# Kernel tuning notes

Hardware: AMD Instinct MI355X
Metric: run time of the kernel (lower is better)

The kernel has to match this reference:

```python
import jax, jax.numpy as jnp
import numpy as np

MODEL_DIM = 1024
HEAD_DIM = 64
NUM_HEADS = 16
FF_DIM = 4 * MODEL_DIM
ROT_DIM = 32  # max(head_dim // 2, 32)
FUSED = (NUM_HEADS * HEAD_DIM,) * 3 + (FF_DIM,) * 2
B, S = 2, 2048


def rotate_half(x):
    x1, x2 = jnp.split(x, 2, axis=-1)
    return jnp.concatenate([-x2, x1], axis=-1)


def rope_freqs(seq_len, dim=ROT_DIM, max_period=10000.0):
    inv_freq = 1.0 / max_period ** (jnp.arange(0, dim, 2, dtype=jnp.float32) / dim)
    freqs = jnp.arange(seq_len, dtype=jnp.float32)[:, None] * inv_freq[None, :]
    return jnp.concatenate([freqs, freqs], axis=-1)  # [S, dim]


def setup_inputs() -> dict:
    key = jax.random.key(0)
    ks = jax.random.split(key, 10)
    d = MODEL_DIM
    s_in = (sum(FUSED) ** -0.5)
    return {
        "inputs": jax.random.normal(ks[0], (B, S, d), jnp.float32),
        "time_embeds": jax.random.normal(ks[1], (B, 1, d), jnp.float32),
        "ln_w": jnp.ones((d,), jnp.float32),
        "ln_b": jnp.zeros((d,), jnp.float32),
        "cond_w": jax.random.normal(ks[2], (d, 2 * d), jnp.float32) * (d ** -0.5),
        "cond_b": jnp.zeros((2 * d,), jnp.float32),
        "w_in": jax.random.normal(ks[3], (d, sum(FUSED)), jnp.float32) * (d ** -0.5),
        "w_attn": jax.random.normal(ks[4], (NUM_HEADS * HEAD_DIM, d), jnp.float32) * ((NUM_HEADS * HEAD_DIM) ** -0.5),
        "w_ff": jax.random.normal(ks[5], (FF_DIM, d), jnp.float32) * (FF_DIM ** -0.5),
        "b_ff": jnp.zeros((d,), jnp.float32),
    }


def reference(inputs, time_embeds, ln_w, ln_b, cond_w, cond_b, w_in, w_attn, w_ff, b_ff):
    # LayerNorm
    mu = jnp.mean(inputs, axis=-1, keepdims=True)
    var = jnp.mean(jnp.square(inputs - mu), axis=-1, keepdims=True)
    units = (inputs - mu) * jax.lax.rsqrt(var + 1e-5) * ln_w + ln_b

    # FiLM conditioning
    cond = jax.nn.silu(time_embeds) @ cond_w + cond_b  # [B,1,2D]
    scale, bias = jnp.split(cond, 2, axis=-1)
    units = (1.0 + scale) * units + bias

    # Fused projection -> q, k, v, ff, ff_gate
    proj = units @ w_in
    splits = np.cumsum(FUSED)[:-1].tolist()
    q, k, v, ff, ff_gate = jnp.split(proj, splits, axis=-1)

    def split_heads(x):  # [B,S,H*hd] -> [B,H,S,hd]
        return x.reshape(B, S, NUM_HEADS, HEAD_DIM).transpose(0, 2, 1, 3)

    q, k, v = split_heads(q), split_heads(k), split_heads(v)

    # Rotary on first ROT_DIM dims of q, k
    freqs = rope_freqs(S)  # [S, ROT_DIM]
    cos, sin = jnp.cos(freqs), jnp.sin(freqs)

    def rope(x):
        xl, xr = x[..., :ROT_DIM], x[..., ROT_DIM:]
        xl = xl * cos + rotate_half(xl) * sin
        return jnp.concatenate([xl, xr], axis=-1)

    q, k = rope(q), rope(k)

    # Attention (full score matrix, manual softmax, as original)
    score = jnp.einsum("bhsd,bhSd->bhsS", q, k) * (HEAD_DIM ** -0.5)
    weight = jax.nn.softmax(score, axis=-1)
    attn = jnp.einsum("bhsS,bhSd->bhsd", weight, v)
    concat = attn.transpose(0, 2, 1, 3).reshape(B, S, NUM_HEADS * HEAD_DIM)
    attn_out = concat @ w_attn

    # GeGLU FF
    ff_out = (ff * jax.nn.gelu(ff_gate, approximate=True)) @ w_ff + b_ff

    return inputs + attn_out + ff_out
```

## Files before the change

kernel.cpp:

```cpp
#include <hip/hip_runtime.h>
#include <hip/hip_bf16.h>

typedef __attribute__((ext_vector_type(8))) __bf16 bf16x8;
typedef __attribute__((ext_vector_type(4))) float f32x4;
typedef unsigned short u16;
typedef unsigned int u32;

#define DMODEL 1024
#define SLEN   2048
#define NPROJ  11264
#define NFUSE  5120
#define MROWS  4096

__device__ __forceinline__ float b2f(u16 u){ u32 v=((u32)u)<<16; float f; __builtin_memcpy(&f,&v,4); return f; }
__device__ __forceinline__ u16 f2b(float f){ u32 u; __builtin_memcpy(&u,&f,4); u32 r=u+0x7fffu+((u>>16)&1u); return (u16)(r>>16); }
__device__ __forceinline__ float fexp2(float x){ return __builtin_amdgcn_exp2f(x); }

__device__ __forceinline__ void gload16(const void* g, void* l){
  __builtin_amdgcn_global_load_lds((__attribute__((address_space(1))) u32*)g,
                                   (__attribute__((address_space(3))) u32*)l, 16, 0, 0);
}

#define BARR asm volatile("s_barrier" ::: "memory")

template<int REMAP>
__global__ __launch_bounds__(256) void k_transpose(const float* __restrict__ src, int N,
                                                   u16* __restrict__ dst, int ldd, int coloff){
  __shared__ float tile[32][33];
  int n0 = blockIdx.x*32, k0 = blockIdx.y*32;
  int tx = threadIdx.x & 31, ty = threadIdx.x >> 5;
  int srccol;
  if (REMAP && (n0 + tx) >= 3072){
    int c = n0 + tx - 3072;
    int q = c >> 5, o = c & 31;
    srccol = (o < 16) ? (3072 + 16*q + o) : (7168 + 16*q + (o-16));
  } else srccol = n0 + tx;
  #pragma unroll
  for (int r=0;r<4;r++)
    tile[ty*4+r][tx] = src[(size_t)(k0+ty*4+r)*N + srccol];
  __syncthreads();
  #pragma unroll
  for (int r=0;r<4;r++){
    int n = ty*4+r;
    dst[(size_t)(n0+n)*ldd + coloff + k0 + tx] = f2b(tile[tx][n]);
  }
}

__global__ __launch_bounds__(256) void k_rope_table(float* __restrict__ tab){
  int idx = blockIdx.x*256 + threadIdx.x;
  if (idx >= SLEN*16) return;
  int s = idx >> 4, i = idx & 15;
  float inv = powf(10000.f, -(float)i/16.f);
  float f = (float)s * inv;
  tab[s*32 + i]      = cosf(f);
  tab[s*32 + 16 + i] = sinf(f);
}

__global__ __launch_bounds__(256) void k_cond(const float* __restrict__ te, const float* __restrict__ cw,
                                              const float* __restrict__ cb, float* __restrict__ cond){
  __shared__ float sl[DMODEL];
  int b = blockIdx.y, t = threadIdx.x;
  for (int i=t;i<DMODEL;i+=256){ float x = te[b*DMODEL+i]; sl[i] = x/(1.f+expf(-x)); }
  __syncthreads();
  int n = blockIdx.x*256 + t;
  float acc = 0.f;
  for (int k=0;k<DMODEL;k++) acc += sl[k]*cw[(size_t)k*2048 + n];
  cond[b*2048+n] = acc + cb[n];
}

__global__ __launch_bounds__(256) void k_ln(const float* __restrict__ x, const float* __restrict__ lw,
                                            const float* __restrict__ lb, const float* __restrict__ cond,
                                            u16* __restrict__ units){
  int row = blockIdx.x; int b = row >> 11;
  int t = threadIdx.x;
  const float4 v = *(const float4*)(x + (size_t)row*DMODEL + t*4);
  float s = v.x+v.y+v.z+v.w;
  float q = v.x*v.x+v.y*v.y+v.z*v.z+v.w*v.w;
  #pragma unroll
  for (int off=32; off; off>>=1){ s += __shfl_xor(s,off); q += __shfl_xor(q,off); }
  __shared__ float red[8];
  int w = t>>6, l = t&63;
  if (l==0){ red[w]=s; red[4+w]=q; }
  __syncthreads();
  float S = red[0]+red[1]+red[2]+red[3];
  float Q = red[4]+red[5]+red[6]+red[7];
  float mu = S*(1.f/1024.f);
  float var = Q*(1.f/1024.f) - mu*mu;
  float rstd = rsqrtf(var + 1e-5f);
  int c0 = t*4;
  u16 o[4];
  const float* vf = (const float*)&v;
  #pragma unroll
  for (int i=0;i<4;i++){
    int c = c0+i;
    float nrm = (vf[i]-mu)*rstd*lw[c] + lb[c];
    float outv = (1.f + cond[b*2048 + c])*nrm + cond[b*2048 + 1024 + c];
    o[i] = f2b(outv);
  }
  u32 p0 = (u32)o[0] | ((u32)o[1]<<16);
  u32 p1 = (u32)o[2] | ((u32)o[3]<<16);
  uint2 pk; pk.x = p0; pk.y = p1;
  *(uint2*)(units + (size_t)row*DMODEL + c0) = pk;
}

__global__ __launch_bounds__(512,2) void k_gemm8_proj(
    const u16* __restrict__ A, const u16* __restrict__ Bt, const float* __restrict__ tab,
    u16* __restrict__ qh, u16* __restrict__ kh, u16* __restrict__ vq, u16* __restrict__ afinal)
{
  __shared__ __attribute__((aligned(16))) u16 lds[65536];
  int t = threadIdx.x, w = t>>6, l = t&63;
  int wr = w>>2, wc = w&3;
  int lane16 = l&15, lg = l>>4;

  int nbx = gridDim.x;
  int wg = blockIdx.y*nbx + blockIdx.x;
  int nwg = nbx*gridDim.y;
  int cpx = nwg>>3;
  int swz = (wg&7)*cpx + (wg>>3);
  int bx = swz % nbx, by = swz / nbx;

  size_t m0 = (size_t)by*256, n0 = (size_t)bx*256;
  const u16* Ag = A + m0*DMODEL;
  const u16* Bg = Bt + n0*DMODEL;

  f32x4 zero = {0.f,0.f,0.f,0.f};
  f32x4 acc[8][4];
  #pragma unroll
  for (int i=0;i<8;i++)
    #pragma unroll
    for (int j=0;j<4;j++) acc[i][j] = zero;

  bf16x8 a[8][2], bv[4][2];

  auto STAGEA = [&](int u, int h){
    const u16* src = Ag + (size_t)(h*128)*DMODEL + u*64;
    char* dst = (char*)lds + ((u&1)<<16) + (h<<14);
    #pragma unroll
    for (int i=0;i<2;i++){
      int cid = i*512 + t;
      int r = cid>>3, s2 = cid&7;
      gload16(src + (size_t)r*DMODEL + ((s2 ^ (r&7))<<3), dst + ((i*512 + w*64)<<4));
    }
  };
  auto STAGEB = [&](int u, int h){
    const u16* src = Bg + (size_t)(h*128)*DMODEL + u*64;
    char* dst = (char*)lds + ((u&1)<<16) + 32768 + (h<<14);
    #pragma unroll
    for (int i=0;i<2;i++){
      int cid = i*512 + t;
      int r = cid>>3, s2 = cid&7;
      gload16(src + (size_t)r*DMODEL + ((s2 ^ (r&7))<<3), dst + ((i*512 + w*64)<<4));
    }
  };
  auto LDA4 = [&](int u, int fi0){
    const char* base = (const char*)lds + ((u&1)<<16) + (wr<<14);
    #pragma unroll
    for (int i=0;i<4;i++){
      int r = (fi0+i)*16 + lane16;
      #pragma unroll
      for (int kk=0;kk<2;kk++){
        int c = kk*4 + lg;
        a[fi0+i][kk] = *(const bf16x8*)(base + r*128 + ((c ^ (r&7))<<4));
      }
    }
  };
  auto LDB2 = [&](int u, int fj0){
    const char* base = (const char*)lds + ((u&1)<<16) + 32768 + ((wc>>1)<<14);
    #pragma unroll
    for (int j=0;j<2;j++){
      int r = (wc&1)*64 + (fj0+j)*16 + lane16;
      #pragma unroll
      for (int kk=0;kk<2;kk++){
        int c = kk*4 + lg;
        bv[fj0+j][kk] = *(const bf16x8*)(base + r*128 + ((c ^ (r&7))<<4));
      }
    }
  };
  auto MMQ = [&](int I0, int J0){
    #pragma unroll
    for (int i=0;i<4;i++)
      #pragma unroll
      for (int j=0;j<2;j++)
        #pragma unroll
        for (int kk=0;kk<2;kk++)
          acc[I0+i][J0+j] = __builtin_amdgcn_mfma_f32_16x16x32_bf16(
              a[I0+i][kk], bv[J0+j][kk], acc[I0+i][J0+j], 0,0,0);
  };

  const int T = DMODEL/64;
  STAGEA(0,0); STAGEA(0,1); STAGEB(0,0); STAGEB(0,1); STAGEA(1,0); STAGEA(1,1);
  asm volatile("s_waitcnt vmcnt(4)" ::: "memory");
  BARR;

  for (int u=0; u<T; ++u){
    LDA4(u,0); LDB2(u,0);
    if (u+1<T) STAGEB(u+1,0);
    BARR;
    __builtin_amdgcn_s_setprio(1);
    MMQ(0,0);
    __builtin_amdgcn_s_setprio(0);
    BARR;
    LDA4(u,4);
    if (u+1<T) STAGEB(u+1,1);
    BARR;
    __builtin_amdgcn_s_setprio(1);
    MMQ(4,0);
    __builtin_amdgcn_s_setprio(0);
    BARR;
    LDB2(u,2);
    if (u+2<T) STAGEA(u+2,0);
    BARR;
    __builtin_amdgcn_s_setprio(1);
    MMQ(0,2);
    __builtin_amdgcn_s_setprio(0);
    BARR;
    if (u+2<T) STAGEA(u+2,1);
    BARR;
    __builtin_amdgcn_s_setprio(1);
    MMQ(4,2);
    __builtin_amdgcn_s_setprio(0);
    asm volatile("s_waitcnt vmcnt(4)" ::: "memory");
    BARR;
  }

  int region = (n0 < 3072) ? (int)(n0>>10) : 3;
  if (region<=1){
    u16* dst = (region==0)? qh : kh;
    float sc = (region==0)? 0.125f*1.44269504f : 1.0f;
    int h = (int)((n0 & 1023)>>6) + wc;
    int d = lane16;
    #pragma unroll
    for (int i=0;i<8;i++){
      #pragma unroll
      for (int r=0;r<4;r++){
        int row = (int)m0 + wr*128 + i*16 + lg*4 + r;
        int bb = row>>11, s = row&2047;
        float cs = tab[s*32+d], sn = tab[s*32+16+d];
        float x0 = acc[i][0][r], x1 = acc[i][1][r];
        size_t base = ((size_t)(bb*16+h)*SLEN + s)*64;
        dst[base+d]    = f2b((x0*cs - x1*sn)*sc);
        dst[base+16+d] = f2b((x1*cs + x0*sn)*sc);
        dst[base+32+d] = f2b(acc[i][2][r]*sc);
        dst[base+48+d] = f2b(acc[i][3][r]*sc);
      }
    }
  } else if (region==2){
    #pragma unroll
    for (int i=0;i<8;i++)
      #pragma unroll
      for (int j=0;j<4;j++){
        int cv = (int)(n0-2048) + wc*64 + j*16 + lane16;
        #pragma unroll
        for (int r=0;r<4;r++){
          int row = (int)m0 + wr*128 + i*16 + lg*4 + r;
          vq[(size_t)row*DMODEL + cv] = f2b(acc[i][j][r]);
        }
      }
  } else {
    int fbase = (int)((n0-3072)>>1) + wc*32 + lane16;
    #pragma unroll
    for (int i=0;i<8;i++)
      #pragma unroll
      for (int p=0;p<2;p++){
        int col = 1024 + fbase + p*16;
        #pragma unroll
        for (int r=0;r<4;r++){
          int row = (int)m0 + wr*128 + i*16 + lg*4 + r;
          float fv = acc[i][2*p][r];
          float gv = acc[i][2*p+1][r];
          float tz = 0.7978845608f*(gv + 0.044715f*gv*gv*gv);
          float th = 1.f - 2.f/(__expf(2.f*tz)+1.f);
          afinal[(size_t)row*NFUSE + col] = f2b(fv * 0.5f*gv*(1.f+th));
        }
      }
  }
}

template<int BM,int BN,int WM,int WN,int NBUF,int MINW,int EPI>
__global__ __launch_bounds__(WM*WN*64, MINW) void k_gemm_pipe(
    const u16* __restrict__ A, const u16* __restrict__ Bt, int K, int lda, int ldb,
    const float* __restrict__ tab, u16* __restrict__ qh, u16* __restrict__ kh,
    u16* __restrict__ vq, u16* __restrict__ afinal, float* __restrict__ pb)
{
  constexpr int THREADS = WM*WN*64;
  constexpr int MR = BM/WM/16, NR = BN/WN/16;
  constexpr int BUFE = (BM+BN)*32;
  __shared__ __attribute__((aligned(16))) u16 lds[NBUF*BUFE];
  int t = threadIdx.x, w = t>>6, l = t&63;
  int wr = w/WN, wc = w%WN;
  int lane16 = l&15, lg = l>>4;

  int nbx = gridDim.x;
  int wg = blockIdx.y*nbx + blockIdx.x;
  int nwg = nbx*gridDim.y;
  int cpx = nwg>>3;
  int swz = (wg&7)*cpx + (wg>>3);
  int bx = swz % nbx, by = swz / nbx;

  size_t m0 = (size_t)by*BM, n0 = (size_t)bx*BN;
  int koff = (EPI==1) ? blockIdx.z*1280 : 0;
  const u16* Ag = A + m0*lda + koff;
  const u16* Bg = Bt + n0*ldb + koff;

  f32x4 zero = {0.f,0.f,0.f,0.f};
  f32x4 acc[MR][NR];
  #pragma unroll
  for (int i=0;i<MR;i++)
    #pragma unroll
    for (int j=0;j<NR;j++) acc[i][j] = zero;

  const int ntiles = K/32;

  auto STAGE = [&](int tt, int buf){
    int k0 = tt*32;
    char* Ad = (char*)lds + (size_t)buf*(BUFE*2);
    char* Bd = Ad + BM*64;
    #pragma unroll
    for (int i=0;i<2;i++){
      int s = i*THREADS + t;
      int r = s>>2, g = s&3;
      int src = (g ^ ((r>>1)&3))*8;
      gload16(Ag + (size_t)r*lda + k0 + src, Ad + (i*THREADS + w*64)*16);
      gload16(Bg + (size_t)r*ldb + k0 + src, Bd + (i*THREADS + w*64)*16);
    }
  };

  #pragma unroll
  for (int p=0;p<NBUF-1;p++) STAGE(p, p);

  int cur = 0;
  for (int kt=0; kt<ntiles; ++kt){
    int rem = ntiles-1-kt;
    if (rem>=1)      asm volatile("s_waitcnt vmcnt(4)" ::: "memory");
    else             asm volatile("s_waitcnt vmcnt(0)" ::: "memory");
    __builtin_amdgcn_s_barrier();
    const u16* As = lds + (size_t)cur*BUFE;
    const u16* Bs = As + BM*32;
    bf16x8 af[MR], bf[NR];
    #pragma unroll
    for (int i=0;i<MR;i++){
      int r = wr*(MR*16) + i*16 + lane16;
      int g = lg ^ ((r>>1)&3);
      af[i] = *(const bf16x8*)(As + r*32 + g*8);
    }
    #pragma unroll
    for (int j=0;j<NR;j++){
      int r = wc*(NR*16) + j*16 + lane16;
      int g = lg ^ ((r>>1)&3);
      bf[j] = *(const bf16x8*)(Bs + r*32 + g*8);
    }
    int st = kt + NBUF-1;
    if (st < ntiles) STAGE(st, (cur==0)?(NBUF-1):(cur-1));
    __builtin_amdgcn_s_setprio(1);
    #pragma unroll
    for (int i=0;i<MR;i++)
      #pragma unroll
      for (int j=0;j<NR;j++)
        acc[i][j] = __builtin_amdgcn_mfma_f32_16x16x32_bf16(af[i], bf[j], acc[i][j], 0,0,0);
    __builtin_amdgcn_s_setprio(0);
    __builtin_amdgcn_sched_barrier(0);
    cur = (cur+1==NBUF)?0:(cur+1);
  }

  if constexpr (EPI==1){
    float* pbs = pb + (size_t)blockIdx.z*MROWS*DMODEL;
    #pragma unroll
    for (int i=0;i<MR;i++)
      #pragma unroll
      for (int j=0;j<NR;j++){
        int col = (int)n0 + wc*(NR*16) + j*16 + lane16;
        #pragma unroll
        for (int r=0;r<4;r++){
          int row = (int)m0 + wr*(MR*16) + i*16 + lg*4 + r;
          pbs[(size_t)row*DMODEL + col] = acc[i][j][r];
        }
      }
  }
}

__global__ __launch_bounds__(256) void k_reduce(const float* __restrict__ pb, const float* __restrict__ resid,
                                                const float* __restrict__ bias, float* __restrict__ out){
  size_t i4 = ((size_t)blockIdx.x*256 + threadIdx.x)*4;
  float4 a0 = *(const float4*)(pb + i4);
  float4 a1 = *(const float4*)(pb + (size_t)MROWS*DMODEL + i4);
  float4 a2 = *(const float4*)(pb + (size_t)2*MROWS*DMODEL + i4);
  float4 a3 = *(const float4*)(pb + (size_t)3*MROWS*DMODEL + i4);
  float4 rv = *(const float4*)(resid + i4);
  float4 bv = *(const float4*)(bias + (i4 & 1023));
  float4 o;
  o.x = a0.x+a1.x+a2.x+a3.x+rv.x+bv.x;
  o.y = a0.y+a1.y+a2.y+a3.y+rv.y+bv.y;
  o.z = a0.z+a1.z+a2.z+a3.z+rv.z+bv.z;
  o.w = a0.w+a1.w+a2.w+a3.w+rv.w+bv.w;
  *(float4*)(out + i4) = o;
}

__global__ __launch_bounds__(256) void k_vtrans(const u16* __restrict__ vq, u16* __restrict__ vt){
  int b = blockIdx.z, h = blockIdx.y, s0 = blockIdx.x*64;
  int t = threadIdx.x;
  __shared__ u16 vt_lds[64][72];
  int sl = t>>2, quad = t&3;
  const u16* prow = vq + (size_t)(b*SLEN + s0 + sl)*DMODEL + h*64;
  #pragma unroll
  for (int i=0;i<16;i++){
    int d = quad*16+i;
    vt_lds[d][sl] = prow[d];
  }
  __syncthreads();
  int d = t>>2, sg = t&3;
  size_t base = ((size_t)(b*16+h)*64 + d)*SLEN + s0 + sg*16;
  #pragma unroll
  for (int i=0;i<16;i++)
    vt[base + i] = vt_lds[d][sg*16+i];
}

#define M0SHIFT 20.0f
__global__ __launch_bounds__(256,3) void k_attn(const u16* __restrict__ qh, const u16* __restrict__ kh,
                                                const u16* __restrict__ vt,
                                                float* __restrict__ op, float* __restrict__ lsum){
  __shared__ __attribute__((aligned(16))) u16 Klds[2][64*64];
  __shared__ __attribute__((aligned(16))) u16 Vlds[2][64*64];
  __shared__ __attribute__((aligned(16))) u16 Plds[4][32*72];
  int p = (blockIdx.z*16 + blockIdx.y)*16 + blockIdx.x;
  int c = p&7, k = p>>3;
  int hb = c + 8*(k&3);
  int rem = k>>2;
  int split = rem>>4, qx = rem&15;
  int b = hb>>4, h = hb&15, q0 = qx*128;
  int kvbase = split*1024;
  int t = threadIdx.x, w = t>>6, l = t&63;
  int lane16 = l&15, lg = l>>4;
  size_t hoff = (size_t)hb*SLEN*64;
  const u16* Qb = qh + hoff + (size_t)(q0 + w*32)*64;
  const u16* Kb = kh + hoff;
  const u16* Vb = vt + hoff;
  bf16x8 qf[2][2];
  #pragma unroll
  for (int mi=0;mi<2;mi++)
    #pragma unroll
    for (int ks=0;ks<2;ks++)
      qf[mi][ks] = *(const bf16x8*)(Qb + (size_t)(mi*16+lane16)*64 + ks*32 + lg*8);
  bf16x8 ones;
  #pragma unroll
  for (int i=0;i<8;i++) ones[i] = (__bf16)1.0f;
  f32x4 zero = {0.f,0.f,0.f,0.f};
  f32x4 acc[2][4];
  f32x4 lacc[2];
  #pragma unroll
  for (int mi=0;mi<2;mi++){
    lacc[mi] = zero;
    #pragma unroll
    for (int n=0;n<4;n++) acc[mi][n] = zero;
  }

  auto STAGE = [&](int buf, int kv0){
    #pragma unroll
    for (int r=0;r<2;r++){
      int cc = r*256 + t;
      int row = cc>>3;
      int g = (cc&7) ^ (row&7);
      gload16(Kb + (size_t)(kv0+row)*64 + g*8, (char*)Klds[buf] + r*4096 + w*1024);
      gload16(Vb + (size_t)row*SLEN + kv0 + g*8, (char*)Vlds[buf] + r*4096 + w*1024);
    }
  };

  STAGE(0, kvbase);
  __syncthreads();

  for (int tile=0; tile<16; ++tile){
    int cur = tile & 1;
    if (tile+1 < 16) STAGE(cur^1, kvbase + (tile+1)*64);
    f32x4 sf[2][4];
    #pragma unroll
    for (int mi=0;mi<2;mi++)
      #pragma unroll
      for (int n=0;n<4;n++) sf[mi][n] = zero;
    __builtin_amdgcn_s_setprio(1);
    #pragma unroll
    for (int n=0;n<4;n++){
      #pragma unroll
      for (int ks=0;ks<2;ks++){
        int rk = n*16 + lane16;
        int g = (ks*4 + lg) ^ (rk&7);
        bf16x8 kf = *(const bf16x8*)(Klds[cur] + rk*64 + g*8);
        sf[0][n] = __builtin_amdgcn_mfma_f32_16x16x32_bf16(qf[0][ks], kf, sf[0][n], 0,0,0);
        sf[1][n] = __builtin_amdgcn_mfma_f32_16x16x32_bf16(qf[1][ks], kf, sf[1][n], 0,0,0);
      }
    }
    __builtin_amdgcn_s_setprio(0);
    #pragma unroll
    for (int mi=0;mi<2;mi++)
      #pragma unroll
      for (int jr=0;jr<4;jr++)
        #pragma unroll
        for (int n=0;n<4;n++){
          float pv = fexp2(sf[mi][n][jr] - M0SHIFT);
          u32 u; __builtin_memcpy(&u,&pv,4);
          Plds[w][(mi*16 + lg*4 + jr)*72 + n*16 + lane16] = (u16)(u>>16);
        }
    __builtin_amdgcn_s_setprio(1);
    #pragma unroll
    for (int ks=0;ks<2;ks++){
      bf16x8 vf[4];
      #pragma unroll
      for (int n=0;n<4;n++){
        int rv = n*16 + lane16;
        int g = (ks*4 + lg) ^ (rv&7);
        vf[n] = *(const bf16x8*)(Vlds[cur] + rv*64 + g*8);
      }
      #pragma unroll
      for (int mi=0;mi<2;mi++){
        bf16x8 pa = *(const bf16x8*)(&Plds[w][(mi*16 + lane16)*72 + ks*32 + lg*8]);
        #pragma unroll
        for (int n=0;n<4;n++)
          acc[mi][n] = __builtin_amdgcn_mfma_f32_16x16x32_bf16(pa, vf[n], acc[mi][n], 0,0,0);
        lacc[mi] = __builtin_amdgcn_mfma_f32_16x16x32_bf16(pa, ones, lacc[mi], 0,0,0);
      }
    }
    __builtin_amdgcn_s_setprio(0);
    __syncthreads();
  }
  float* ops = op + (size_t)split*MROWS*DMODEL;
  #pragma unroll
  for (int mi=0;mi<2;mi++)
    #pragma unroll
    for (int n=0;n<4;n++)
      #pragma unroll
      for (int jr=0;jr<4;jr++){
        int srow = q0 + w*32 + mi*16 + lg*4 + jr;
        size_t r = (size_t)b*SLEN + srow;
        ops[r*DMODEL + h*64 + n*16 + lane16] = acc[mi][n][jr];
      }
  if (lane16==0){
    #pragma unroll
    for (int mi=0;mi<2;mi++)
      #pragma unroll
      for (int jr=0;jr<4;jr++){
        int srow = q0 + w*32 + mi*16 + lg*4 + jr;
        size_t r = (size_t)b*SLEN + srow;
        lsum[((size_t)split*MROWS + r)*16 + h] = lacc[mi][jr];
      }
  }
}

__global__ __launch_bounds__(256) void k_attn_combine(const float* __restrict__ op,
                                                      const float* __restrict__ lsum,
                                                      u16* __restrict__ afinal){
  size_t i4 = ((size_t)blockIdx.x*256 + threadIdx.x)*4;
  int r = (int)(i4>>10), col = (int)(i4&1023), h = col>>6;
  float l0 = lsum[(size_t)r*16+h];
  float l1 = lsum[((size_t)MROWS + r)*16 + h];
  float inv = 1.f/(l0 + l1);
  float4 o0 = *(const float4*)(op + i4);
  float4 o1 = *(const float4*)(op + (size_t)MROWS*DMODEL + i4);
  union { u16 o[4]; uint2 v; } res;
  res.o[0] = f2b((o0.x + o1.x)*inv);
  res.o[1] = f2b((o0.y + o1.y)*inv);
  res.o[2] = f2b((o0.z + o1.z)*inv);
  res.o[3] = f2b((o0.w + o1.w)*inv);
  *(uint2*)(afinal + (size_t)r*NFUSE + col) = res.v;
}

extern "C" void kernel_launch(void* const* d_in, const int* in_sizes, int n_in,
                              void* d_out, int out_size, void* d_ws, size_t ws_size,
                              hipStream_t stream) {
  const float* inputs = (const float*)d_in[0];
  const float* te     = (const float*)d_in[1];
  const float* ln_w   = (const float*)d_in[2];
  const float* ln_b   = (const float*)d_in[3];
  const float* cond_w = (const float*)d_in[4];
  const float* cond_b = (const float*)d_in[5];
  const float* w_in   = (const float*)d_in[6];
  const float* w_attn = (const float*)d_in[7];
  const float* w_ff   = (const float*)d_in[8];
  const float* b_ff   = (const float*)d_in[9];
  float* out = (float*)d_out;

  char* ws = (char*)d_ws;
  size_t off = 0;
  auto alloc = [&](size_t n)->char*{ char* p = ws + off; off += (n + 255) & ~(size_t)255; return p; };
  u16*  w_inT    = (u16*)alloc((size_t)NPROJ*DMODEL*2);
  u16*  w_fusedT = (u16*)alloc((size_t)DMODEL*NFUSE*2);
  u16*  units    = (u16*)alloc((size_t)MROWS*DMODEL*2);
  u16*  qh       = (u16*)alloc((size_t)MROWS*DMODEL*2);
  u16*  kh       = (u16*)alloc((size_t)MROWS*DMODEL*2);
  u16*  vq       = (u16*)alloc((size_t)MROWS*DMODEL*2);
  u16*  vT       = (u16*)alloc((size_t)MROWS*DMODEL*2);
  u16*  afinal   = (u16*)alloc((size_t)MROWS*NFUSE*2);
  float* pb      = (float*)alloc((size_t)4*MROWS*DMODEL*4);
  float* lsum    = (float*)alloc((size_t)2*MROWS*16*4);
  float* cond    = (float*)alloc(2*2048*4);
  float* ropetab = (float*)alloc((size_t)SLEN*32*4);
  float* op      = pb;
  (void)ws_size; (void)in_sizes; (void)n_in; (void)out_size;

  k_transpose<1><<<dim3(NPROJ/32, DMODEL/32), 256, 0, stream>>>(w_in, NPROJ, w_inT, DMODEL, 0);
  k_transpose<0><<<dim3(DMODEL/32, DMODEL/32), 256, 0, stream>>>(w_attn, DMODEL, w_fusedT, NFUSE, 0);
  k_transpose<0><<<dim3(DMODEL/32, 4096/32), 256, 0, stream>>>(w_ff, DMODEL, w_fusedT, NFUSE, DMODEL);
  k_rope_table<<<128, 256, 0, stream>>>(ropetab);
  k_cond<<<dim3(8,2), 256, 0, stream>>>(te, cond_w, cond_b, cond);
  k_ln<<<MROWS, 256, 0, stream>>>(inputs, ln_w, ln_b, cond, units);
  k_gemm8_proj<<<dim3(NPROJ/256, MROWS/256), 512, 0, stream>>>(units, w_inT, ropetab, qh, kh, vq, afinal);
  k_vtrans<<<dim3(SLEN/64, 16, 2), 256, 0, stream>>>(vq, vT);
  k_attn<<<dim3(16, 16, 4), 256, 0, stream>>>(qh, kh, vT, op, lsum);
  k_attn_combine<<<dim3(MROWS*DMODEL/1024), 256, 0, stream>>>(op, lsum, afinal);
  k_gemm_pipe<128,128,2,2,3,3,1><<<dim3(DMODEL/128, MROWS/128, 4), 256, 0, stream>>>(
      afinal, w_fusedT, 1280, NFUSE, NFUSE, nullptr, nullptr, nullptr, nullptr, nullptr, pb);
  k_reduce<<<dim3(MROWS*DMODEL/1024), 256, 0, stream>>>(pb, inputs, b_ff, out);
}
```

Baseline: 321.8 us.

## Drop KV split in attention, fuse normalization, halve output GEMM split-K

Attention now processes the full KV length in one block and normalizes and writes bf16 directly into the fused activation buffer, which removes the separate combine kernel and the fp32 partial output traffic. The output GEMM split-K goes from 4 to 2, so fewer fp32 partials are written and read by the reduce. It also changes the proj GEMM tile mapping from modulo/divide to shift/mask, which assumes a fixed grid shape. The cost is half as many attention and GEMM workgroups, which lowers parallelism and lengthens each block's serial loop.

Result: faster. 293.8 us (-8.7%).

```diff
diff --git a/kernel.cpp b/kernel.cpp
--- a/kernel.cpp
+++ b/kernel.cpp
@@ -117,7 +117,7 @@
   int nwg = nbx*gridDim.y;
   int cpx = nwg>>3;
   int swz = (wg&7)*cpx + (wg>>3);
-  int bx = swz % nbx, by = swz / nbx;
+  int bx = swz >> 4, by = swz & 15;
 
   size_t m0 = (size_t)by*256, n0 = (size_t)bx*256;
   const u16* Ag = A + m0*DMODEL;
@@ -298,7 +298,7 @@
   int bx = swz % nbx, by = swz / nbx;
 
   size_t m0 = (size_t)by*BM, n0 = (size_t)bx*BN;
-  int koff = (EPI==1) ? blockIdx.z*1280 : 0;
+  int koff = (EPI==1) ? blockIdx.z*2560 : 0;
   const u16* Ag = A + m0*lda + koff;
   const u16* Bg = Bt + n0*ldb + koff;
 
@@ -383,15 +383,13 @@
   size_t i4 = ((size_t)blockIdx.x*256 + threadIdx.x)*4;
   float4 a0 = *(const float4*)(pb + i4);
   float4 a1 = *(const float4*)(pb + (size_t)MROWS*DMODEL + i4);
-  float4 a2 = *(const float4*)(pb + (size_t)2*MROWS*DMODEL + i4);
-  float4 a3 = *(const float4*)(pb + (size_t)3*MROWS*DMODEL + i4);
   float4 rv = *(const float4*)(resid + i4);
   float4 bv = *(const float4*)(bias + (i4 & 1023));
   float4 o;
-  o.x = a0.x+a1.x+a2.x+a3.x+rv.x+bv.x;
-  o.y = a0.y+a1.y+a2.y+a3.y+rv.y+bv.y;
-  o.z = a0.z+a1.z+a2.z+a3.z+rv.z+bv.z;
-  o.w = a0.w+a1.w+a2.w+a3.w+rv.w+bv.w;
+  o.x = a0.x+a1.x+rv.x+bv.x;
+  o.y = a0.y+a1.y+rv.y+bv.y;
+  o.z = a0.z+a1.z+rv.z+bv.z;
+  o.w = a0.w+a1.w+rv.w+bv.w;
   *(float4*)(out + i4) = o;
 }
 
@@ -416,18 +414,15 @@
 
 #define M0SHIFT 20.0f
 __global__ __launch_bounds__(256,3) void k_attn(const u16* __restrict__ qh, const u16* __restrict__ kh,
-                                                const u16* __restrict__ vt,
-                                                float* __restrict__ op, float* __restrict__ lsum){
+                                                const u16* __restrict__ vt, u16* __restrict__ afinal){
   __shared__ __attribute__((aligned(16))) u16 Klds[2][64*64];
   __shared__ __attribute__((aligned(16))) u16 Vlds[2][64*64];
   __shared__ __attribute__((aligned(16))) u16 Plds[4][32*72];
   int p = (blockIdx.z*16 + blockIdx.y)*16 + blockIdx.x;
   int c = p&7, k = p>>3;
   int hb = c + 8*(k&3);
-  int rem = k>>2;
-  int split = rem>>4, qx = rem&15;
+  int qx = k>>2;
   int b = hb>>4, h = hb&15, q0 = qx*128;
-  int kvbase = split*1024;
   int t = threadIdx.x, w = t>>6, l = t&63;
   int lane16 = l&15, lg = l>>4;
   size_t hoff = (size_t)hb*SLEN*64;
@@ -464,12 +459,12 @@
     }
   };
 
-  STAGE(0, kvbase);
+  STAGE(0, 0);
   __syncthreads();
 
-  for (int tile=0; tile<16; ++tile){
+  for (int tile=0; tile<32; ++tile){
     int cur = tile & 1;
-    if (tile+1 < 16) STAGE(cur^1, kvbase + (tile+1)*64);
+    if (tile+1 < 32) STAGE(cur^1, (tile+1)*64);
     f32x4 sf[2][4];
     #pragma unroll
     for (int mi=0;mi<2;mi++)
@@ -520,45 +515,20 @@
     __builtin_amdgcn_s_setprio(0);
     __syncthreads();
   }
-  float* ops = op + (size_t)split*MROWS*DMODEL;
-  #pragma unroll
-  for (int mi=0;mi<2;mi++)
+  #pragma unroll
+  for (int mi=0;mi<2;mi++){
+    float inv[4];
+    #pragma unroll
+    for (int jr=0;jr<4;jr++) inv[jr] = 1.f/lacc[mi][jr];
     #pragma unroll
     for (int n=0;n<4;n++)
       #pragma unroll
       for (int jr=0;jr<4;jr++){
         int srow = q0 + w*32 + mi*16 + lg*4 + jr;
-        size_t r = (size_t)b*SLEN + srow;
-        ops[r*DMODEL + h*64 + n*16 + lane16] = acc[mi][n][jr];
-      }
-  if (lane16==0){
-    #pragma unroll
-    for (int mi=0;mi<2;mi++)
-      #pragma unroll
-      for (int jr=0;jr<4;jr++){
-        int srow = q0 + w*32 + mi*16 + lg*4 + jr;
-        size_t r = (size_t)b*SLEN + srow;
-        lsum[((size_t)split*MROWS + r)*16 + h] = lacc[mi][jr];
-      }
-  }
-}
-
-__global__ __launch_bounds__(256) void k_attn_combine(const float* __restrict__ op,
-                                                      const float* __restrict__ lsum,
-                                                      u16* __restrict__ afinal){
-  size_t i4 = ((size_t)blockIdx.x*256 + threadIdx.x)*4;
-  int r = (int)(i4>>10), col = (int)(i4&1023), h = col>>6;
-  float l0 = lsum[(size_t)r*16+h];
-  float l1 = lsum[((size_t)MROWS + r)*16 + h];
-  float inv = 1.f/(l0 + l1);
-  float4 o0 = *(const float4*)(op + i4);
-  float4 o1 = *(const float4*)(op + (size_t)MROWS*DMODEL + i4);
-  union { u16 o[4]; uint2 v; } res;
-  res.o[0] = f2b((o0.x + o1.x)*inv);
-  res.o[1] = f2b((o0.y + o1.y)*inv);
-  res.o[2] = f2b((o0.z + o1.z)*inv);
-  res.o[3] = f2b((o0.w + o1.w)*inv);
-  *(uint2*)(afinal + (size_t)r*NFUSE + col) = res.v;
+        int col = h*64 + n*16 + lane16;
+        afinal[(size_t)(b*SLEN+srow)*NFUSE + col] = f2b(acc[mi][n][jr]*inv[jr]);
+      }
+  }
 }
 
 extern "C" void kernel_launch(void* const* d_in, const int* in_sizes, int n_in,
@@ -587,11 +557,9 @@
   u16*  vq       = (u16*)alloc((size_t)MROWS*DMODEL*2);
   u16*  vT       = (u16*)alloc((size_t)MROWS*DMODEL*2);
   u16*  afinal   = (u16*)alloc((size_t)MROWS*NFUSE*2);
-  float* pb      = (float*)alloc((size_t)4*MROWS*DMODEL*4);
-  float* lsum    = (float*)alloc((size_t)2*MROWS*16*4);
+  float* pb      = (float*)alloc((size_t)2*MROWS*DMODEL*4);
   float* cond    = (float*)alloc(2*2048*4);
   float* ropetab = (float*)alloc((size_t)SLEN*32*4);
-  float* op      = pb;
   (void)ws_size; (void)in_sizes; (void)n_in; (void)out_size;
 
   k_transpose<1><<<dim3(NPROJ/32, DMODEL/32), 256, 0, stream>>>(w_in, NPROJ, w_inT, DMODEL, 0);
@@ -602,9 +570,8 @@
   k_ln<<<MROWS, 256, 0, stream>>>(inputs, ln_w, ln_b, cond, units);
   k_gemm8_proj<<<dim3(NPROJ/256, MROWS/256), 512, 0, stream>>>(units, w_inT, ropetab, qh, kh, vq, afinal);
   k_vtrans<<<dim3(SLEN/64, 16, 2), 256, 0, stream>>>(vq, vT);
-  k_attn<<<dim3(16, 16, 4), 256, 0, stream>>>(qh, kh, vT, op, lsum);
-  k_attn_combine<<<dim3(MROWS*DMODEL/1024), 256, 0, stream>>>(op, lsum, afinal);
-  k_gemm_pipe<128,128,2,2,3,3,1><<<dim3(DMODEL/128, MROWS/128, 4), 256, 0, stream>>>(
-      afinal, w_fusedT, 1280, NFUSE, NFUSE, nullptr, nullptr, nullptr, nullptr, nullptr, pb);
+  k_attn<<<dim3(16, 16, 2), 256, 0, stream>>>(qh, kh, vT, afinal);
+  k_gemm_pipe<128,128,2,2,3,3,1><<<dim3(DMODEL/128, MROWS/128, 2), 256, 0, stream>>>(
+      afinal, w_fusedT, 2560, NFUSE, NFUSE, nullptr, nullptr, nullptr, nullptr, nullptr, pb);
   k_reduce<<<dim3(MROWS*DMODEL/1024), 256, 0, stream>>>(pb, inputs, b_ff, out);
 }
```
